# Optimization experiments

Measured on AMD Instinct MI355X. Metric: run time of the kernel, lower is better.

## Reference

```python
import jax, jax.numpy as jnp
import numpy as np

N_SRC, N_DST, K, T = 16384, 8192, 16, 2
NODE_IN, EDGE_IN, TIME_D = 128, 64, 128
D_MODEL = NODE_IN + TIME_D + EDGE_IN  # 320
N_HEAD, D_K = 8, 64                   # d_k = d_v
HID = 128
LN_EPS = 1e-5


def setup_inputs() -> dict:
    key = jax.random.key(0)
    ks = jax.random.split(key, 10)
    std_qk = np.sqrt(2.0 / (D_MODEL + D_K)).astype(np.float32)
    return {
        "node_features": jax.random.normal(ks[0], (N_SRC, NODE_IN), jnp.float32),
        "edge_features": jax.random.normal(ks[1], (N_DST, K, T, EDGE_IN), jnp.float32),
        "delta_t": jax.random.uniform(ks[2], (N_DST, K, T), jnp.float32) * 100.0,
        "neigh_idx": jax.random.randint(ks[3], (N_DST, K), 0, N_SRC),
        "basis_freq": jnp.asarray(1.0 / 10 ** np.linspace(0, 9, TIME_D), jnp.float32),
        "phase": jnp.zeros((TIME_D,), jnp.float32),
        "w_qs": jax.random.normal(ks[4], (N_HEAD * D_K, D_MODEL), jnp.float32) * std_qk,
        "w_ks": jax.random.normal(ks[5], (N_HEAD * D_K, D_MODEL), jnp.float32) * std_qk,
        "w_vs": jax.random.normal(ks[6], (N_HEAD * D_K, D_MODEL), jnp.float32) * std_qk,
        "fc_w": jax.random.normal(ks[7], (D_MODEL, N_HEAD * D_K), jnp.float32) * 0.03,
        "fc_b": jnp.zeros((D_MODEL,), jnp.float32),
        "ln_g": jnp.ones((D_MODEL,), jnp.float32),
        "ln_b": jnp.zeros((D_MODEL,), jnp.float32),
        "node_w": jax.random.normal(ks[8], (HID, 2 * NODE_IN + TIME_D + EDGE_IN), jnp.float32) * 0.05,
        "node_b": jnp.zeros((HID,), jnp.float32),
    }


def reference(node_features, edge_features, delta_t, neigh_idx, basis_freq, phase,
              w_qs, w_ks, w_vs, fc_w, fc_b, ln_g, ln_b, node_w, node_b):
    h_dst = node_features[:N_DST]                                  # [N, NODE_IN]
    # message_func: per-edge time encoding + gather src feats + concat
    te = jnp.cos(delta_t[..., None] * basis_freq + phase)          # [N, K, T, TIME_D]
    h_nb = node_features[neigh_idx]                                # [N, K, NODE_IN] (irregular gather)
    h_nb = jnp.broadcast_to(h_nb[:, :, None, :], (N_DST, K, T, NODE_IN))
    m = jnp.concatenate([h_nb, edge_features, te], axis=-1)        # [N, K, T, D_MODEL]
    m = m.reshape(N_DST, K * T, D_MODEL)                           # mailbox kv
    # reduce_func query: [h_dst, zeros(edge_in), time_encode(0)=cos(phase)]
    t0 = jnp.broadcast_to(jnp.cos(phase), (N_DST, TIME_D))
    q = jnp.concatenate([h_dst, jnp.zeros((N_DST, EDGE_IN), h_dst.dtype), t0], axis=-1)  # [N, D_MODEL]
    # multi-head attention (len_q = 1)
    qh = (q @ w_qs.T).reshape(N_DST, N_HEAD, D_K)
    kh = (m @ w_ks.T).reshape(N_DST, K * T, N_HEAD, D_K)
    vh = (m @ w_vs.T).reshape(N_DST, K * T, N_HEAD, D_K)
    scores = jnp.einsum('nhd,nlhd->nhl', qh, kh) / np.float32(np.sqrt(D_K))
    attn = jax.nn.softmax(scores, axis=-1)
    ctx = jnp.einsum('nhl,nlhd->nhd', attn, vh).reshape(N_DST, N_HEAD * D_K)
    out = ctx @ fc_w.T + fc_b
    x = out + q                                                    # residual
    mu = x.mean(-1, keepdims=True)
    var = x.var(-1, keepdims=True)
    h_neigh = ln_g * (x - mu) * jax.lax.rsqrt(var + LN_EPS) + ln_b  # layer norm
    h = jnp.concatenate([h_dst, h_neigh], axis=-1)                 # [N, 2*NODE_IN+TIME_D+EDGE_IN]
    return jax.nn.relu(h @ node_w.T + node_b)                      # [N, HID]
```

## Files before the change

### kernel.cpp

```cpp
#include <hip/hip_runtime.h>
#include <math.h>

#define LNB      32
#define NODE_IN  128
#define EDGE_IN  64
#define TIME_D   128
#define D_MODEL  320
#define N_HEAD   8
#define D_K      64
#define NHD      512
#define HID      128
#define IN2      448
#define N_DSTN   8192

typedef __attribute__((ext_vector_type(8))) short bf16x8;
typedef __attribute__((ext_vector_type(4))) float f32x4;
#define MFMA16(a,b,c) __builtin_amdgcn_mfma_f32_16x16x32_bf16(a,b,c,0,0,0)

#define WS_QKM   0
#define WS_WQK   20971520
#define WS_WVF   21299200
#define WS_NWC   22118400
#define WS_F32   22175744
#define WS_X     22182784

#define F_C0     0
#define F_C0K    512
#define F_CC     3072
#define F_B2     3392

__device__ __forceinline__ unsigned short f2bf(float f) {
  union { float f; unsigned i; } v; v.f = f;
  unsigned x = v.i;
  return (unsigned short)((x + 0x7fffu + ((x >> 16) & 1u)) >> 16);
}
__device__ __forceinline__ bf16x8 pack8(const float* v) {
  unsigned short b8[8];
  #pragma unroll
  for (int j = 0; j < 8; ++j) b8[j] = f2bf(v[j]);
  return *(const bf16x8*)b8;
}

__global__ __launch_bounds__(256)
void prep1a(const float* __restrict__ nw, const float* __restrict__ lng,
            const float* __restrict__ fcb, const float* __restrict__ ph,
            unsigned short* __restrict__ ws)
{
  int i = blockIdx.x * 256 + threadIdx.x;
  unsigned short* nwc = ws + WS_NWC;
  float* f32r = (float*)(ws + WS_F32);
  if (i < 16384) {
    int o = i >> 7, k = i & 127;
    nwc[o * IN2 + k] = f2bf(nw[(size_t)o * IN2 + k]);
  } else if (i < 57344) {
    int j = i - 16384, o = j / 320, c = j - o * 320;
    nwc[o * IN2 + 128 + c] = f2bf(nw[(size_t)o * IN2 + 128 + c] * lng[c]);
  } else if (i < 57664) {
    int c = i - 57344;
    f32r[F_CC + c] = fcb[c] + (c >= 192 ? __cosf(ph[c - 192]) : 0.f);
  }
}

__global__ __launch_bounds__(256)
void prep1b(const float* __restrict__ wq, const float* __restrict__ ph,
            const float* __restrict__ nw, const float* __restrict__ lnb_,
            const float* __restrict__ nb, unsigned short* __restrict__ ws)
{
  float* f32r = (float*)(ws + WS_F32);
  int gw = (blockIdx.x * 256 + threadIdx.x) >> 6;
  int ln = threadIdx.x & 63;
  if (gw < 512) {
    float s = __cosf(ph[ln])      * wq[(size_t)gw * D_MODEL + 192 + ln]
            + __cosf(ph[ln + 64]) * wq[(size_t)gw * D_MODEL + 256 + ln];
    #pragma unroll
    for (int off = 32; off >= 1; off >>= 1) s += __shfl_xor(s, off);
    if (ln == 0) f32r[F_C0 + gw] = s;
  } else {
    int o = gw - 512;
    float s = 0.f;
    #pragma unroll
    for (int k = 0; k < 5; ++k) {
      int c = ln + 64 * k;
      s += nw[(size_t)o * IN2 + 128 + c] * lnb_[c];
    }
    #pragma unroll
    for (int off = 32; off >= 1; off >>= 1) s += __shfl_xor(s, off);
    if (ln == 0) f32r[F_B2 + o] = nb[o] + s;
  }
}

__global__ __launch_bounds__(256)
void prep_c0k(const float* __restrict__ wk, unsigned short* __restrict__ ws)
{
  float* f32r = (float*)(ws + WS_F32);
  int gw = (blockIdx.x * 256 + threadIdx.x) >> 6;
  int ln = threadIdx.x & 63;
  int h = gw / 320, d = gw - h * 320;
  float s = f32r[F_C0 + h * 64 + ln] * wk[(size_t)(h * 64 + ln) * D_MODEL + d];
  #pragma unroll
  for (int off = 32; off >= 1; off >>= 1) s += __shfl_xor(s, off);
  if (ln == 0) f32r[F_C0K + gw] = s;
}

__global__ __launch_bounds__(256)
void prep_wqk(const float* __restrict__ wq, const float* __restrict__ wk,
              unsigned short* __restrict__ ws)
{
  __shared__ float sQw[64 * 128];
  __shared__ float sKw[64 * 32];
  int h = blockIdx.x / 10, d0 = (blockIdx.x - h * 10) * 32;
  int tid = threadIdx.x;
  #pragma unroll 4
  for (int it = 0; it < 32; ++it) {
    int idx = it * 256 + tid;
    int r = idx >> 7, c = idx & 127;
    sQw[idx] = wq[(size_t)(h * 64 + r) * D_MODEL + c];
  }
  #pragma unroll
  for (int it = 0; it < 8; ++it) {
    int idx = it * 256 + tid;
    int r = idx >> 5, c = idx & 31;
    sKw[idx] = wk[(size_t)(h * 64 + r) * D_MODEL + d0 + c];
  }
  __syncthreads();
  int di = tid >> 3, k0 = (tid & 7) * 16;
  float acc[16] = {};
  for (int dk = 0; dk < 64; ++dk) {
    float w = sKw[dk * 32 + di];
    #pragma unroll
    for (int j = 0; j < 16; ++j) acc[j] += w * sQw[dk * 128 + k0 + j];
  }
  unsigned short* dst = ws + WS_WQK + (size_t)(h * 320 + d0 + di) * 128 + k0;
  #pragma unroll
  for (int j = 0; j < 16; ++j) dst[j] = f2bf(acc[j]);
}

__global__ __launch_bounds__(256)
void prep_wvf(const float* __restrict__ fcw, const float* __restrict__ wv,
              unsigned short* __restrict__ ws)
{
  __shared__ float sF[32 * 64];
  __shared__ float sW[64 * 32];
  int b = blockIdx.x;
  int h = b / 100, r2 = b - h * 100;
  int ct = r2 / 10;
  int c0 = ct * 32, d0 = (r2 - ct * 10) * 32;
  int tid = threadIdx.x;
  #pragma unroll
  for (int it = 0; it < 8; ++it) {
    int idx = it * 256 + tid;
    int i = idx >> 6, jj = idx & 63;
    sF[idx] = fcw[(size_t)(c0 + i) * NHD + h * 64 + jj];
  }
  #pragma unroll
  for (int it = 0; it < 8; ++it) {
    int idx = it * 256 + tid;
    int jj = idx >> 5, i = idx & 31;
    sW[idx] = wv[(size_t)(h * 64 + jj) * D_MODEL + d0 + i];
  }
  __syncthreads();
  int ci = tid >> 3, dj0 = (tid & 7) * 4;
  float acc[4] = {};
  for (int jj = 0; jj < 64; ++jj) {
    float f = sF[ci * 64 + jj];
    #pragma unroll
    for (int k = 0; k < 4; ++k) acc[k] += f * sW[jj * 32 + dj0 + k];
  }
  unsigned short* wvf = ws + WS_WVF;
  #pragma unroll
  for (int k = 0; k < 4; ++k)
    wvf[(size_t)(c0 + ci) * 2560 + (size_t)(d0 + dj0 + k) * 8 + h] = f2bf(acc[k]);
}

__global__ __launch_bounds__(256, 6)
void tgat_qk(const float* __restrict__ nf, const unsigned short* __restrict__ ws,
             unsigned short* __restrict__ qkm)
{
  __shared__ alignas(16) unsigned short sA[64 * 136];
  const int tid = threadIdx.x, wid = tid >> 6, lane = tid & 63, qd = lane >> 4, lm = lane & 15;
  const int mt_blk = blockIdx.x / 20, nt_blk = blockIdx.x - mt_blk * 20;
  const int n0 = mt_blk * 64, c0 = nt_blk * 128;
  const unsigned short* wqk = ws + WS_WQK;
  const float* f32r = (const float*)(ws + WS_F32);

  {
    int n = tid >> 2, k0 = (tid & 3) * 32;
    const float4* src = (const float4*)(nf + (size_t)(n0 + n) * NODE_IN + k0);
    #pragma unroll
    for (int q = 0; q < 4; ++q) {
      float4 f0 = src[2 * q], f1 = src[2 * q + 1];
      float v[8] = {f0.x, f0.y, f0.z, f0.w, f1.x, f1.y, f1.z, f1.w};
      *(bf16x8*)&sA[n * 136 + k0 + q * 8] = pack8(v);
    }
  }
  __syncthreads();

  f32x4 acc[2][4] = {};
  for (int kt = 0; kt < 4; ++kt) {
    bf16x8 a[4];
    #pragma unroll
    for (int mt = 0; mt < 4; ++mt)
      a[mt] = *(const bf16x8*)&sA[(mt * 16 + lm) * 136 + kt * 32 + qd * 8];
    #pragma unroll
    for (int t = 0; t < 2; ++t) {
      int cg = c0 + (2 * wid + t) * 16 + lm;
      bf16x8 b = *(const bf16x8*)&wqk[(size_t)cg * 128 + kt * 32 + qd * 8];
      #pragma unroll
      for (int mt = 0; mt < 4; ++mt) acc[t][mt] = MFMA16(a[mt], b, acc[t][mt]);
    }
  }
  #pragma unroll
  for (int t = 0; t < 2; ++t) {
    int cg = c0 + (2 * wid + t) * 16 + lm;
    float ck = f32r[F_C0K + cg];
    #pragma unroll
    for (int mt = 0; mt < 4; ++mt)
      #pragma unroll
      for (int r = 0; r < 4; ++r)
        qkm[(size_t)(n0 + mt * 16 + qd * 4 + r) * 2560 + cg] = f2bf(acc[t][mt][r] + ck);
  }
}

__global__ __launch_bounds__(256, 5)
void tgat_attn(const float* __restrict__ nf, const float* __restrict__ ef,
               const float* __restrict__ dtp, const int* __restrict__ nidx,
               const float* __restrict__ freq, const float* __restrict__ ph,
               unsigned short* __restrict__ qkm)
{
  __shared__ alignas(16) unsigned short sM[LNB * 328];
  __shared__ alignas(16) unsigned short sQN[8 * 328];
  __shared__ alignas(16) unsigned short sATT[16 * 40];
  __shared__ float sFP[TIME_D], sPH[TIME_D], sDT[LNB];
  __shared__ int   sNI[16];

  const int tid = threadIdx.x;
  const int wid = tid >> 6, lane = tid & 63, qd = lane >> 4, lm = lane & 15;
  const int n = blockIdx.x;
  unsigned short* qn = qkm + (size_t)n * 2560;

  if (tid < TIME_D) { sFP[tid] = freq[tid]; sPH[tid] = ph[tid]; }
  if (tid < 16)  sNI[tid] = nidx[n * 16 + tid];
  if (tid < LNB) sDT[tid] = dtp[(size_t)n * LNB + tid];
  if (tid >= 64 && tid < 192) {
    for (int j = tid - 64; j < 320; j += 128) {
      int r = j / 40, c8 = j - r * 40;
      *(bf16x8*)&sQN[r * 328 + c8 * 8] = *(const bf16x8*)&qn[r * 320 + c8 * 8];
    }
  }
  __syncthreads();

  #pragma unroll 1
  for (int it = 0; it < 5; ++it) {
    int g = it * 256 + tid;
    int l = g & 31, dg = g >> 5;
    int d0 = dg * 8;
    float v[8];
    if (dg < 16) {
      const float4* src = (const float4*)(nf + (size_t)sNI[l >> 1] * NODE_IN + d0);
      float4 f0 = src[0], f1 = src[1];
      v[0]=f0.x; v[1]=f0.y; v[2]=f0.z; v[3]=f0.w; v[4]=f1.x; v[5]=f1.y; v[6]=f1.z; v[7]=f1.w;
    } else if (dg < 24) {
      const float4* src = (const float4*)(ef + ((size_t)n * LNB + l) * EDGE_IN + (d0 - NODE_IN));
      float4 f0 = src[0], f1 = src[1];
      v[0]=f0.x; v[1]=f0.y; v[2]=f0.z; v[3]=f0.w; v[4]=f1.x; v[5]=f1.y; v[6]=f1.z; v[7]=f1.w;
    } else {
      int dd = d0 - 192;
      float dt = sDT[l];
      #pragma unroll
      for (int j = 0; j < 8; ++j) v[j] = __cosf(dt * sFP[dd + j] + sPH[dd + j]);
    }
    *(bf16x8*)&sM[l * 328 + d0] = pack8(v);
  }
  __syncthreads();

  if (wid == 0) {
    f32x4 acc0 = {}, acc1 = {};
    for (int kt = 0; kt < 10; ++kt) {
      bf16x8 b = {0,0,0,0,0,0,0,0};
      if (lm < 8) b = *(const bf16x8*)&sQN[lm * 328 + kt * 32 + qd * 8];
      bf16x8 a0 = *(const bf16x8*)&sM[lm * 328 + kt * 32 + qd * 8];
      bf16x8 a1 = *(const bf16x8*)&sM[(16 + lm) * 328 + kt * 32 + qd * 8];
      acc0 = MFMA16(a0, b, acc0);
      acc1 = MFMA16(a1, b, acc1);
    }
    float s[8], e[8];
    #pragma unroll
    for (int r = 0; r < 4; ++r) { s[r] = acc0[r] * 0.125f; s[4 + r] = acc1[r] * 0.125f; }
    float mx = s[0];
    #pragma unroll
    for (int i = 1; i < 8; ++i) mx = fmaxf(mx, s[i]);
    mx = fmaxf(mx, __shfl_xor(mx, 16));
    mx = fmaxf(mx, __shfl_xor(mx, 32));
    float sum = 0.f;
    #pragma unroll
    for (int i = 0; i < 8; ++i) { e[i] = __expf(s[i] - mx); sum += e[i]; }
    sum += __shfl_xor(sum, 16);
    sum += __shfl_xor(sum, 32);
    float inv = 1.f / sum;
    #pragma unroll
    for (int i = 0; i < 8; ++i) {
      int l = (i < 4) ? (qd * 4 + i) : (16 + qd * 4 + (i - 4));
      sATT[lm * 40 + l] = f2bf(e[i] * inv);
    }
  }
  __syncthreads();

  {
    bf16x8 batt = *(const bf16x8*)&sATT[lm * 40 + qd * 8];
    #pragma unroll
    for (int w = 0; w < 5; ++w) {
      int dt = wid * 5 + w;
      int d = dt * 16 + lm;
      unsigned short a8[8];
      #pragma unroll
      for (int j = 0; j < 8; ++j) a8[j] = sM[(qd * 8 + j) * 328 + d];
      f32x4 acc = {};
      acc = MFMA16(*(const bf16x8*)a8, batt, acc);
      if (lm < 8) {
        #pragma unroll
        for (int r = 0; r < 4; ++r)
          qn[(dt * 16 + qd * 4 + r) * 8 + lm] = f2bf(acc[r]);
      }
    }
  }
}

__global__ __launch_bounds__(256)
void tgat_xgemm(const unsigned short* __restrict__ ws,
                const unsigned short* __restrict__ qkm, float* __restrict__ xacc)
{
  __shared__ alignas(16) unsigned short sA[64 * 136];
  const int tid = threadIdx.x, wid = tid >> 6, lane = tid & 63, qd = lane >> 4, lm = lane & 15;
  const int s = blockIdx.x >> 7, mb = blockIdx.x & 127;
  const int n0 = mb * 64, k0 = s * 640;
  const unsigned short* wvf = ws + WS_WVF;

  f32x4 acc[4][5] = {};
  for (int kc = 0; kc < 5; ++kc) {
    __syncthreads();
    {
      int n = tid >> 2, p = (tid & 3) * 32;
      const unsigned short* src = qkm + (size_t)(n0 + n) * 2560 + k0 + kc * 128 + p;
      *(bf16x8*)&sA[n * 136 + p]      = *(const bf16x8*)(src);
      *(bf16x8*)&sA[n * 136 + p + 8]  = *(const bf16x8*)(src + 8);
      *(bf16x8*)&sA[n * 136 + p + 16] = *(const bf16x8*)(src + 16);
      *(bf16x8*)&sA[n * 136 + p + 24] = *(const bf16x8*)(src + 24);
    }
    __syncthreads();
    #pragma unroll
    for (int kt = 0; kt < 4; ++kt) {
      bf16x8 b[5];
      #pragma unroll
      for (int u = 0; u < 5; ++u) {
        int c = wid * 80 + u * 16 + lm;
        b[u] = *(const bf16x8*)&wvf[(size_t)c * 2560 + k0 + kc * 128 + kt * 32 + qd * 8];
      }
      #pragma unroll
      for (int mt = 0; mt < 4; ++mt) {
        bf16x8 a = *(const bf16x8*)&sA[(mt * 16 + lm) * 136 + kt * 32 + qd * 8];
        #pragma unroll
        for (int u = 0; u < 5; ++u) acc[mt][u] = MFMA16(a, b[u], acc[mt][u]);
      }
    }
  }
  #pragma unroll
  for (int mt = 0; mt < 4; ++mt)
    #pragma unroll
    for (int u = 0; u < 5; ++u) {
      int c = wid * 80 + u * 16 + lm;
      #pragma unroll
      for (int r = 0; r < 4; ++r)
        atomicAdd(&xacc[(size_t)(n0 + mt * 16 + qd * 4 + r) * 320 + c], acc[mt][u][r]);
    }
}

__global__ __launch_bounds__(256, 4)
void tgat_post2(const float* __restrict__ nf, const unsigned short* __restrict__ ws,
                const float* __restrict__ xacc, float* __restrict__ out)
{
  __shared__ alignas(16) unsigned short sQb[16 * 136];
  __shared__ alignas(16) unsigned short sXb[16 * 328];
  const int tid = threadIdx.x, wid = tid >> 6, lane = tid & 63, qd = lane >> 4, lm = lane & 15;
  const int n0 = blockIdx.x * 16;
  const unsigned short* nwc = ws + WS_NWC;
  const float* f32r = (const float*)(ws + WS_F32);

  {
    int nn = tid >> 4, kk = (tid & 15) * 8;
    const float4* src = (const float4*)(nf + (size_t)(n0 + nn) * NODE_IN + kk);
    float4 f0 = src[0], f1 = src[1];
    float v8[8] = {f0.x, f0.y, f0.z, f0.w, f1.x, f1.y, f1.z, f1.w};
    *(bf16x8*)&sQb[nn * 136 + kk] = pack8(v8);
  }
  const int rr = tid >> 4, cl = tid & 15;
  float v[20], s1 = 0.f, s2 = 0.f;
  #pragma unroll
  for (int u = 0; u < 20; ++u) {
    int c = u * 16 + cl;
    float x = xacc[(size_t)(n0 + rr) * 320 + c] + f32r[F_CC + c];
    if (c < 128) x += nf[(size_t)(n0 + rr) * NODE_IN + c];
    v[u] = x; s1 += x; s2 += x * x;
  }
  #pragma unroll
  for (int off = 8; off >= 1; off >>= 1) { s1 += __shfl_xor(s1, off); s2 += __shfl_xor(s2, off); }
  float mean = s1 * (1.f / D_MODEL);
  float var  = s2 * (1.f / D_MODEL) - mean * mean;
  float rstd = rsqrtf(var + 1e-5f);
  #pragma unroll
  for (int u = 0; u < 20; ++u) {
    int c = u * 16 + cl;
    sXb[rr * 328 + c] = f2bf((v[u] - mean) * rstd);
  }
  __syncthreads();

  #pragma unroll
  for (int t = 0; t < 2; ++t) {
    int o = (wid * 2 + t) * 16 + lm;
    f32x4 acc = {};
    for (int kt = 0; kt < 14; ++kt) {
      bf16x8 a;
      if (kt < 4) a = *(const bf16x8*)&sQb[lm * 136 + kt * 32 + qd * 8];
      else        a = *(const bf16x8*)&sXb[lm * 328 + (kt - 4) * 32 + qd * 8];
      bf16x8 b = *(const bf16x8*)&nwc[(size_t)o * IN2 + kt * 32 + qd * 8];
      acc = MFMA16(a, b, acc);
    }
    float bz = f32r[F_B2 + o];
    #pragma unroll
    for (int r = 0; r < 4; ++r)
      out[(size_t)(n0 + qd * 4 + r) * HID + o] = fmaxf(acc[r] + bz, 0.f);
  }
}

extern "C" void kernel_launch(void* const* d_in, const int* in_sizes, int n_in,
                              void* d_out, int out_size, void* d_ws, size_t ws_size,
                              hipStream_t stream) {
  const float* nf   = (const float*)d_in[0];
  const float* ef   = (const float*)d_in[1];
  const float* dtp  = (const float*)d_in[2];
  const int*   nidx = (const int*)  d_in[3];
  const float* freq = (const float*)d_in[4];
  const float* ph   = (const float*)d_in[5];
  const float* wq   = (const float*)d_in[6];
  const float* wk   = (const float*)d_in[7];
  const float* wv   = (const float*)d_in[8];
  const float* fcw  = (const float*)d_in[9];
  const float* fcb  = (const float*)d_in[10];
  const float* lng  = (const float*)d_in[11];
  const float* lnb_ = (const float*)d_in[12];
  const float* nw   = (const float*)d_in[13];
  const float* nb   = (const float*)d_in[14];
  float* out = (float*)d_out;
  unsigned short* ws = (unsigned short*)d_ws;
  unsigned short* qkm = ws + WS_QKM;
  float* xacc = (float*)(ws + WS_X);

  hipMemsetAsync(xacc, 0, (size_t)N_DSTN * D_MODEL * sizeof(float), stream);
  prep1a  <<<226, 256, 0, stream>>>(nw, lng, fcb, ph, ws);
  prep1b  <<<160, 256, 0, stream>>>(wq, ph, nw, lnb_, nb, ws);
  prep_c0k<<<640, 256, 0, stream>>>(wk, ws);
  prep_wqk<<<80,  256, 0, stream>>>(wq, wk, ws);
  prep_wvf<<<800, 256, 0, stream>>>(fcw, wv, ws);
  tgat_qk   <<<2560, 256, 0, stream>>>(nf, ws, qkm);
  tgat_attn <<<8192, 256, 0, stream>>>(nf, ef, dtp, nidx, freq, ph, qkm);
  tgat_xgemm<<<512,  256, 0, stream>>>(ws, qkm, xacc);
  tgat_post2<<<512,  256, 0, stream>>>(nf, ws, xacc, out);
}
```

Before: 284.4 us.

## Overlap attention score softmax with V-fragment loads and drop staging LDS

The attention kernel no longer stages neighbor indices, time-encoding params and the q-projected row in shared memory. It reads them directly from global memory, and wave 0 keeps the query fragments in registers. Waves 1-3 preload their transposed message fragments while wave 0 computes scores and softmax, and the output tiles are rebalanced so wave 0 does 2 tiles and the others do 6. The change also uses the native bf16 conversion and raises the occupancy hint to 6 blocks, which trades more global reads and register pressure for fewer barriers and less LDS.

```diff
diff --git a/kernel.cpp b/kernel.cpp
--- a/kernel.cpp
+++ b/kernel.cpp
@@ -30,9 +30,8 @@
 #define F_B2     3392
 
 __device__ __forceinline__ unsigned short f2bf(float f) {
-  union { float f; unsigned i; } v; v.f = f;
-  unsigned x = v.i;
-  return (unsigned short)((x + 0x7fffu + ((x >> 16) & 1u)) >> 16);
+  __bf16 h = (__bf16)f;
+  return __builtin_bit_cast(unsigned short, h);
 }
 __device__ __forceinline__ bf16x8 pack8(const float* v) {
   unsigned short b8[8];
@@ -221,33 +220,19 @@
   }
 }
 
-__global__ __launch_bounds__(256, 5)
+__global__ __launch_bounds__(256, 6)
 void tgat_attn(const float* __restrict__ nf, const float* __restrict__ ef,
                const float* __restrict__ dtp, const int* __restrict__ nidx,
                const float* __restrict__ freq, const float* __restrict__ ph,
                unsigned short* __restrict__ qkm)
 {
   __shared__ alignas(16) unsigned short sM[LNB * 328];
-  __shared__ alignas(16) unsigned short sQN[8 * 328];
   __shared__ alignas(16) unsigned short sATT[16 * 40];
-  __shared__ float sFP[TIME_D], sPH[TIME_D], sDT[LNB];
-  __shared__ int   sNI[16];
 
   const int tid = threadIdx.x;
   const int wid = tid >> 6, lane = tid & 63, qd = lane >> 4, lm = lane & 15;
   const int n = blockIdx.x;
   unsigned short* qn = qkm + (size_t)n * 2560;
-
-  if (tid < TIME_D) { sFP[tid] = freq[tid]; sPH[tid] = ph[tid]; }
-  if (tid < 16)  sNI[tid] = nidx[n * 16 + tid];
-  if (tid < LNB) sDT[tid] = dtp[(size_t)n * LNB + tid];
-  if (tid >= 64 && tid < 192) {
-    for (int j = tid - 64; j < 320; j += 128) {
-      int r = j / 40, c8 = j - r * 40;
-      *(bf16x8*)&sQN[r * 328 + c8 * 8] = *(const bf16x8*)&qn[r * 320 + c8 * 8];
-    }
-  }
-  __syncthreads();
 
   #pragma unroll 1
   for (int it = 0; it < 5; ++it) {
@@ -256,7 +241,8 @@
     int d0 = dg * 8;
     float v[8];
     if (dg < 16) {
-      const float4* src = (const float4*)(nf + (size_t)sNI[l >> 1] * NODE_IN + d0);
+      int ni = nidx[n * 16 + (l >> 1)];
+      const float4* src = (const float4*)(nf + (size_t)ni * NODE_IN + d0);
       float4 f0 = src[0], f1 = src[1];
       v[0]=f0.x; v[1]=f0.y; v[2]=f0.z; v[3]=f0.w; v[4]=f1.x; v[5]=f1.y; v[6]=f1.z; v[7]=f1.w;
     } else if (dg < 24) {
@@ -265,23 +251,40 @@
       v[0]=f0.x; v[1]=f0.y; v[2]=f0.z; v[3]=f0.w; v[4]=f1.x; v[5]=f1.y; v[6]=f1.z; v[7]=f1.w;
     } else {
       int dd = d0 - 192;
-      float dt = sDT[l];
-      #pragma unroll
-      for (int j = 0; j < 8; ++j) v[j] = __cosf(dt * sFP[dd + j] + sPH[dd + j]);
+      float dt = dtp[(size_t)n * LNB + l];
+      const float4* fq = (const float4*)(freq + dd);
+      const float4* pp = (const float4*)(ph + dd);
+      float4 q0 = fq[0], q1 = fq[1], p0 = pp[0], p1 = pp[1];
+      v[0] = __cosf(dt * q0.x + p0.x); v[1] = __cosf(dt * q0.y + p0.y);
+      v[2] = __cosf(dt * q0.z + p0.z); v[3] = __cosf(dt * q0.w + p0.w);
+      v[4] = __cosf(dt * q1.x + p1.x); v[5] = __cosf(dt * q1.y + p1.y);
+      v[6] = __cosf(dt * q1.z + p1.z); v[7] = __cosf(dt * q1.w + p1.w);
     }
     *(bf16x8*)&sM[l * 328 + d0] = pack8(v);
   }
-  __syncthreads();
+
+  bf16x8 qfrag[10];
+  if (wid == 0) {
+    #pragma unroll
+    for (int kt = 0; kt < 10; ++kt) {
+      qfrag[kt] = (bf16x8){0,0,0,0,0,0,0,0};
+      if (lm < 8) qfrag[kt] = *(const bf16x8*)&qn[lm * 320 + kt * 32 + qd * 8];
+    }
+  }
+  __syncthreads();
+
+  const int tbeg = (wid == 0) ? 0 : 2 + (wid - 1) * 6;
+  const int tcnt = (wid == 0) ? 2 : 6;
+  bf16x8 afr[6];
 
   if (wid == 0) {
     f32x4 acc0 = {}, acc1 = {};
+    #pragma unroll
     for (int kt = 0; kt < 10; ++kt) {
-      bf16x8 b = {0,0,0,0,0,0,0,0};
-      if (lm < 8) b = *(const bf16x8*)&sQN[lm * 328 + kt * 32 + qd * 8];
       bf16x8 a0 = *(const bf16x8*)&sM[lm * 328 + kt * 32 + qd * 8];
       bf16x8 a1 = *(const bf16x8*)&sM[(16 + lm) * 328 + kt * 32 + qd * 8];
-      acc0 = MFMA16(a0, b, acc0);
-      acc1 = MFMA16(a1, b, acc1);
+      acc0 = MFMA16(a0, qfrag[kt], acc0);
+      acc1 = MFMA16(a1, qfrag[kt], acc1);
     }
     float s[8], e[8];
     #pragma unroll
@@ -302,24 +305,39 @@
       int l = (i < 4) ? (qd * 4 + i) : (16 + qd * 4 + (i - 4));
       sATT[lm * 40 + l] = f2bf(e[i] * inv);
     }
-  }
-  __syncthreads();
-
-  {
-    bf16x8 batt = *(const bf16x8*)&sATT[lm * 40 + qd * 8];
-    #pragma unroll
-    for (int w = 0; w < 5; ++w) {
-      int dt = wid * 5 + w;
-      int d = dt * 16 + lm;
+  } else {
+    #pragma unroll
+    for (int u = 0; u < 6; ++u) {
+      int d = (tbeg + u) * 16 + lm;
       unsigned short a8[8];
       #pragma unroll
       for (int j = 0; j < 8; ++j) a8[j] = sM[(qd * 8 + j) * 328 + d];
+      afr[u] = *(const bf16x8*)a8;
+    }
+  }
+  __syncthreads();
+
+  if (wid == 0) {
+    #pragma unroll
+    for (int u = 0; u < 2; ++u) {
+      int d = u * 16 + lm;
+      unsigned short a8[8];
+      #pragma unroll
+      for (int j = 0; j < 8; ++j) a8[j] = sM[(qd * 8 + j) * 328 + d];
+      afr[u] = *(const bf16x8*)a8;
+    }
+  }
+  bf16x8 batt = *(const bf16x8*)&sATT[lm * 40 + qd * 8];
+  #pragma unroll
+  for (int u = 0; u < 6; ++u) {
+    if (u < tcnt) {
+      int dtile = tbeg + u;
       f32x4 acc = {};
-      acc = MFMA16(*(const bf16x8*)a8, batt, acc);
+      acc = MFMA16(afr[u], batt, acc);
       if (lm < 8) {
         #pragma unroll
         for (int r = 0; r < 4; ++r)
-          qn[(dt * 16 + qd * 4 + r) * 8 + lm] = f2bf(acc[r]);
+          qn[(dtile * 16 + qd * 4 + r) * 8 + lm] = f2bf(acc[r]);
       }
     }
   }
```

Result: no change. 283.5 us (-0.3%).
